# Optimization experiments

Hardware: AMD Instinct MI355X
Metric: run time of the kernel (lower is better)

## Reference

```python
import jax, jax.numpy as jnp
import numpy as np


def _bce_per_sample(logits, t):
    # numerically-stable BCE-with-logits, reduced to one scalar per sample
    elem = jnp.maximum(logits, 0.0) - logits * t + jnp.log1p(jnp.exp(-jnp.abs(logits)))
    return jnp.mean(elem, axis=(1, 2, 3))  # [B]


def setup_inputs() -> dict:
    key = jax.random.key(0)
    k1, k2 = jax.random.split(key)
    inputs = jax.random.normal(k1, (8, 1, 224, 224), dtype=jnp.float32)
    targets = jax.random.uniform(k2, (8, 1, 240, 240), dtype=jnp.float32)
    return {"inputs": inputs, "targets": targets}


def reference(inputs, targets):
    B, C, h, w = inputs.shape
    H, W = targets.shape[-2], targets.shape[-1]
    s1 = H - h + 1
    s2 = W - w + 1
    S = s1 * s2

    flat_idx = jnp.arange(S)

    def window(k):
        i = k // s2
        j = k % s2
        return jax.lax.dynamic_slice(targets, (0, 0, i, j), (B, C, h, w))

    # all candidate shifted windows: [S, B, C, h, w]
    windows = jax.vmap(window)(flat_idx)

    # per-shift, per-sample loss (computed without grad in original): [S, B]
    errs = jax.vmap(lambda wdw: _bce_per_sample(inputs, wdw))(windows)

    min_ij = jnp.argmin(errs, axis=0)  # [B] best shift per sample
    adjusted = jax.lax.stop_gradient(windows[min_ij, jnp.arange(B)])  # [B, C, h, w]

    total_loss = jnp.sum(_bce_per_sample(inputs, adjusted))
    return total_loss, adjusted
```

## Files before the change

### kernel.cpp

```cpp
#include <hip/hip_runtime.h>
#include <float.h>

#define H_IN 224
#define W_IN 224
#define H_T  240
#define W_T  240
#define S1   17
#define S2   17
#define NS   (S1*S2)
#define NB   8
#define NPIX (H_IN*W_IN)
#define TPIX (H_T*W_T)
#define ROWG 4
#define ROWS_PER_BLOCK (H_IN/ROWG)
#define ROWS_PER_WAVE  (ROWS_PER_BLOCK/4)
#define PB   (NPIX/256)

#define WS_PART  0
#define WS_FPART 9248

__global__ __launch_bounds__(256) void corr_f_kernel(const float* __restrict__ logits,
                                                     const float* __restrict__ targ,
                                                     float* __restrict__ ws) {
    int bid  = blockIdx.x;
    int rg   = bid % ROWG;
    int i    = (bid / ROWG) % S1;
    int b    = bid / (ROWG * S1);
    int tid  = threadIdx.x;
    int lane = tid & 63;
    int w    = tid >> 6;
    bool active = lane < (W_IN / 4);

    float acc[S2];
#pragma unroll
    for (int j = 0; j < S2; ++j) acc[j] = 0.f;
    float fs = 0.f;

    const float* Lb = logits + b * NPIX;
    const float* Tb = targ   + b * TPIX;
    const int y0 = rg * ROWS_PER_BLOCK + w * ROWS_PER_WAVE;
    const bool do_f = (i == 0);

    for (int r = 0; r < ROWS_PER_WAVE; ++r) {
        int y = y0 + r;
        if (active) {
            const float4 l4 = *(const float4*)(Lb + y * W_IN + lane * 4);
            const float* Tr = Tb + (y + i) * W_T + lane * 4;
            float4 t0 = *(const float4*)(Tr);
            float4 t1 = *(const float4*)(Tr + 4);
            float4 t2 = *(const float4*)(Tr + 8);
            float4 t3 = *(const float4*)(Tr + 12);
            float4 t4 = *(const float4*)(Tr + 16);
            float t[20] = {t0.x,t0.y,t0.z,t0.w, t1.x,t1.y,t1.z,t1.w,
                           t2.x,t2.y,t2.z,t2.w, t3.x,t3.y,t3.z,t3.w,
                           t4.x,t4.y,t4.z,t4.w};
            float l[4] = {l4.x, l4.y, l4.z, l4.w};
#pragma unroll
            for (int j = 0; j < S2; ++j) {
                float s = acc[j];
                s = fmaf(l[0], t[j],     s);
                s = fmaf(l[1], t[j + 1], s);
                s = fmaf(l[2], t[j + 2], s);
                s = fmaf(l[3], t[j + 3], s);
                acc[j] = s;
            }
            if (do_f) {
#pragma unroll
                for (int u = 0; u < 4; ++u) {
                    float v = l[u];
                    fs += fmaxf(v, 0.f) + __logf(1.f + __expf(-fabsf(v)));
                }
            }
        }
    }

#pragma unroll
    for (int j = 0; j < S2; ++j) {
        float v = acc[j];
#pragma unroll
        for (int off = 32; off > 0; off >>= 1)
            v += __shfl_xor(v, off, 64);
        acc[j] = v;
    }

    __shared__ float red[4][S2];
    __shared__ float redf[4];
    if (lane == 0) {
#pragma unroll
        for (int j = 0; j < S2; ++j) red[w][j] = acc[j];
    }
    if (do_f) {
#pragma unroll
        for (int off = 32; off > 0; off >>= 1)
            fs += __shfl_xor(fs, off, 64);
        if (lane == 0) redf[w] = fs;
    }
    __syncthreads();
    if (tid < S2) {
        float v = red[0][tid] + red[1][tid] + red[2][tid] + red[3][tid];
        ws[WS_PART + ((b * S1 + i) * ROWG + rg) * S2 + tid] = v;
    }
    if (do_f && tid == 0)
        ws[WS_FPART + b * ROWG + rg] = redf[0] + redf[1] + redf[2] + redf[3];
}

__device__ __forceinline__ void argmax_for(const float* __restrict__ part, int bb,
                                           int tid, int lane, int w,
                                           float* s_v, int* s_i,
                                           float& o_v, int& o_i) {
    float bv = -FLT_MAX;
    int   bs = NS;
    for (int s = tid; s < NS; s += 256) {
        const float* pp = part + ((bb * S1 + s / S2) * ROWG) * S2 + (s % S2);
        float v = pp[0] + pp[S2] + pp[2 * S2] + pp[3 * S2];
        if (v > bv) { bv = v; bs = s; }
    }
#pragma unroll
    for (int off = 32; off > 0; off >>= 1) {
        float ov = __shfl_down(bv, off, 64);
        int   oi = __shfl_down(bs, off, 64);
        if (ov > bv || (ov == bv && oi < bs)) { bv = ov; bs = oi; }
    }
    if (lane == 0) { s_v[w] = bv; s_i[w] = bs; }
    __syncthreads();
    if (tid == 0) {
        float fv = s_v[0]; int fi = s_i[0];
#pragma unroll
        for (int k = 1; k < 4; ++k) {
            if (s_v[k] > fv || (s_v[k] == fv && s_i[k] < fi)) { fv = s_v[k]; fi = s_i[k]; }
        }
        s_v[4] = fv; s_i[4] = fi;
    }
    __syncthreads();
    o_v = s_v[4];
    o_i = s_i[4];
}

__global__ __launch_bounds__(256) void finish_kernel(const float* __restrict__ targ,
                                                     const float* __restrict__ ws,
                                                     float* __restrict__ out) {
    int blk = blockIdx.x;
    int p   = blk % PB;
    int b   = blk / PB;
    int tid = threadIdx.x;
    int lane = tid & 63;
    int w    = tid >> 6;

    const float* part  = ws + WS_PART;
    const float* fpart = ws + WS_FPART;

    __shared__ float s_v[5];
    __shared__ int   s_i[5];
    __shared__ float s_v8[NB];
    __shared__ int   s_i8[NB];

    float bv; int best;
    if (blk == 0) {
#pragma unroll
        for (int pass = 0; pass < 2; ++pass) {
            int bb = w + pass * 4;
            float bv2 = -FLT_MAX;
            int   bs2 = NS;
            for (int s = lane; s < NS; s += 64) {
                const float* pp = part + ((bb * S1 + s / S2) * ROWG) * S2 + (s % S2);
                float v = pp[0] + pp[S2] + pp[2 * S2] + pp[3 * S2];
                if (v > bv2) { bv2 = v; bs2 = s; }
            }
#pragma unroll
            for (int off = 32; off > 0; off >>= 1) {
                float ov = __shfl_down(bv2, off, 64);
                int   oi = __shfl_down(bs2, off, 64);
                if (ov > bv2 || (ov == bv2 && oi < bs2)) { bv2 = ov; bs2 = oi; }
            }
            if (lane == 0) { s_v8[bb] = bv2; s_i8[bb] = bs2; }
        }
        __syncthreads();
        if (tid == 0) {
            float total = 0.f;
#pragma unroll
            for (int bb = 0; bb < NB; ++bb) {
                float F = fpart[bb * ROWG] + fpart[bb * ROWG + 1] +
                          fpart[bb * ROWG + 2] + fpart[bb * ROWG + 3];
                total += (F - s_v8[bb]) * (1.0f / (float)NPIX);
            }
            out[0] = total;
        }
        best = s_i8[0];
    } else {
        argmax_for(part, b, tid, lane, w, s_v, s_i, bv, best);
    }

    int pix = p * 256 + tid;
    int y = pix / W_IN;
    int x = pix - y * W_IN;
    int i = best / S2;
    int j = best - i * S2;
    out[1 + b * NPIX + pix] = targ[b * TPIX + (y + i) * W_T + (x + j)];
}

extern "C" void kernel_launch(void* const* d_in, const int* in_sizes, int n_in,
                              void* d_out, int out_size, void* d_ws, size_t ws_size,
                              hipStream_t stream) {
    const float* logits = (const float*)d_in[0];
    const float* targ   = (const float*)d_in[1];
    float* out = (float*)d_out;
    float* ws  = (float*)d_ws;

    corr_f_kernel<<<NB * S1 * ROWG, 256, 0, stream>>>(logits, targ, ws);
    finish_kernel<<<NB * PB, 256, 0, stream>>>(targ, ws, out);
}
```

Measured before the change: 25.91 us.

## Fuse correlation and finish kernels via cooperative launch with grid sync

Merges the two kernels into one cooperative kernel with 544 blocks. A grid-wide sync separates the correlation phase from the argmax and gather phase, and each block then copies a chunk of the selected target window. This removes the second kernel launch and its gap, at the cost of a grid barrier and a fixed block count for the copy phase. If the cooperative launch fails, it falls back to the original two-kernel path.

```diff
diff --git a/kernel.cpp b/kernel.cpp
--- a/kernel.cpp
+++ b/kernel.cpp
@@ -1,5 +1,8 @@
 #include <hip/hip_runtime.h>
+#include <hip/hip_cooperative_groups.h>
 #include <float.h>
+
+namespace cg = cooperative_groups;
 
 #define H_IN 224
 #define W_IN 224
@@ -15,20 +18,16 @@
 #define ROWS_PER_BLOCK (H_IN/ROWG)
 #define ROWS_PER_WAVE  (ROWS_PER_BLOCK/4)
 #define PB   (NPIX/256)
+#define QB   (S1*ROWG)
+#define CHUNK 738
 
 #define WS_PART  0
 #define WS_FPART 9248
 
-__global__ __launch_bounds__(256) void corr_f_kernel(const float* __restrict__ logits,
-                                                     const float* __restrict__ targ,
-                                                     float* __restrict__ ws) {
-    int bid  = blockIdx.x;
-    int rg   = bid % ROWG;
-    int i    = (bid / ROWG) % S1;
-    int b    = bid / (ROWG * S1);
-    int tid  = threadIdx.x;
-    int lane = tid & 63;
-    int w    = tid >> 6;
+__device__ __forceinline__ void corr_phase(const float* __restrict__ logits,
+                                           const float* __restrict__ targ,
+                                           float* __restrict__ ws,
+                                           int b, int i, int rg, int tid, int lane, int w) {
     bool active = lane < (W_IN / 4);
 
     float acc[S2];
@@ -136,6 +135,100 @@
     o_i = s_i[4];
 }
 
+__device__ __forceinline__ void argmax_all8(const float* __restrict__ part,
+                                            int lane, int w,
+                                            float* s_v8, int* s_i8) {
+#pragma unroll
+    for (int pass = 0; pass < 2; ++pass) {
+        int bb = w + pass * 4;
+        float bv2 = -FLT_MAX;
+        int   bs2 = NS;
+        for (int s = lane; s < NS; s += 64) {
+            const float* pp = part + ((bb * S1 + s / S2) * ROWG) * S2 + (s % S2);
+            float v = pp[0] + pp[S2] + pp[2 * S2] + pp[3 * S2];
+            if (v > bv2) { bv2 = v; bs2 = s; }
+        }
+#pragma unroll
+        for (int off = 32; off > 0; off >>= 1) {
+            float ov = __shfl_down(bv2, off, 64);
+            int   oi = __shfl_down(bs2, off, 64);
+            if (ov > bv2 || (ov == bv2 && oi < bs2)) { bv2 = ov; bs2 = oi; }
+        }
+        if (lane == 0) { s_v8[bb] = bv2; s_i8[bb] = bs2; }
+    }
+    __syncthreads();
+}
+
+__global__ __launch_bounds__(256, 3) void fused_kernel(const float* __restrict__ logits,
+                                                       const float* __restrict__ targ,
+                                                       float* __restrict__ ws,
+                                                       float* __restrict__ out) {
+    int bid  = blockIdx.x;
+    int rg   = bid % ROWG;
+    int i    = (bid / ROWG) % S1;
+    int b    = bid / QB;
+    int q    = bid - b * QB;
+    int tid  = threadIdx.x;
+    int lane = tid & 63;
+    int w    = tid >> 6;
+
+    corr_phase(logits, targ, ws, b, i, rg, tid, lane, w);
+
+    cg::this_grid().sync();
+
+    const float* part  = ws + WS_PART;
+    const float* fpart = ws + WS_FPART;
+
+    __shared__ float s_v[5];
+    __shared__ int   s_i[5];
+    __shared__ float s_v8[NB];
+    __shared__ int   s_i8[NB];
+
+    int best;
+    if (bid == 0) {
+        argmax_all8(part, lane, w, s_v8, s_i8);
+        if (tid == 0) {
+            float total = 0.f;
+#pragma unroll
+            for (int bb = 0; bb < NB; ++bb) {
+                float F = fpart[bb * ROWG] + fpart[bb * ROWG + 1] +
+                          fpart[bb * ROWG + 2] + fpart[bb * ROWG + 3];
+                total += (F - s_v8[bb]) * (1.0f / (float)NPIX);
+            }
+            out[0] = total;
+        }
+        best = s_i8[0];
+    } else {
+        float bv;
+        argmax_for(part, b, tid, lane, w, s_v, s_i, bv, best);
+    }
+
+    int ii = best / S2;
+    int jj = best - ii * S2;
+    int start = q * CHUNK;
+    int end   = start + CHUNK; if (end > NPIX) end = NPIX;
+    const float* Tb = targ + b * TPIX;
+    float* Ob = out + 1 + b * NPIX;
+    for (int pix = start + tid; pix < end; pix += 256) {
+        int y = pix / W_IN;
+        int x = pix - y * W_IN;
+        Ob[pix] = Tb[(y + ii) * W_T + (x + jj)];
+    }
+}
+
+__global__ __launch_bounds__(256) void corr_f_kernel(const float* __restrict__ logits,
+                                                     const float* __restrict__ targ,
+                                                     float* __restrict__ ws) {
+    int bid  = blockIdx.x;
+    int rg   = bid % ROWG;
+    int i    = (bid / ROWG) % S1;
+    int b    = bid / (ROWG * S1);
+    int tid  = threadIdx.x;
+    int lane = tid & 63;
+    int w    = tid >> 6;
+    corr_phase(logits, targ, ws, b, i, rg, tid, lane, w);
+}
+
 __global__ __launch_bounds__(256) void finish_kernel(const float* __restrict__ targ,
                                                      const float* __restrict__ ws,
                                                      float* __restrict__ out) {
@@ -154,27 +247,9 @@
     __shared__ float s_v8[NB];
     __shared__ int   s_i8[NB];
 
-    float bv; int best;
+    int best;
     if (blk == 0) {
-#pragma unroll
-        for (int pass = 0; pass < 2; ++pass) {
-            int bb = w + pass * 4;
-            float bv2 = -FLT_MAX;
-            int   bs2 = NS;
-            for (int s = lane; s < NS; s += 64) {
-                const float* pp = part + ((bb * S1 + s / S2) * ROWG) * S2 + (s % S2);
-                float v = pp[0] + pp[S2] + pp[2 * S2] + pp[3 * S2];
-                if (v > bv2) { bv2 = v; bs2 = s; }
-            }
-#pragma unroll
-            for (int off = 32; off > 0; off >>= 1) {
-                float ov = __shfl_down(bv2, off, 64);
-                int   oi = __shfl_down(bs2, off, 64);
-                if (ov > bv2 || (ov == bv2 && oi < bs2)) { bv2 = ov; bs2 = oi; }
-            }
-            if (lane == 0) { s_v8[bb] = bv2; s_i8[bb] = bs2; }
-        }
-        __syncthreads();
+        argmax_all8(part, lane, w, s_v8, s_i8);
         if (tid == 0) {
             float total = 0.f;
 #pragma unroll
@@ -187,6 +262,7 @@
         }
         best = s_i8[0];
     } else {
+        float bv;
         argmax_for(part, b, tid, lane, w, s_v, s_i, bv, best);
     }
 
@@ -206,6 +282,13 @@
     float* out = (float*)d_out;
     float* ws  = (float*)d_ws;
 
-    corr_f_kernel<<<NB * S1 * ROWG, 256, 0, stream>>>(logits, targ, ws);
-    finish_kernel<<<NB * PB, 256, 0, stream>>>(targ, ws, out);
-}
+    void* args[] = {(void*)&logits, (void*)&targ, (void*)&ws, (void*)&out};
+    hipError_t err = hipLaunchCooperativeKernel((const void*)fused_kernel,
+                                                dim3(NB * QB), dim3(256),
+                                                args, 0, stream);
+    if (err != hipSuccess) {
+        (void)hipGetLastError();
+        corr_f_kernel<<<NB * S1 * ROWG, 256, 0, stream>>>(logits, targ, ws);
+        finish_kernel<<<NB * PB, 256, 0, stream>>>(targ, ws, out);
+    }
+}
```

New measurement: 74.17 us. 186% more time.
